# Optimization experiments

Hardware: AMD Instinct MI355X
Metric: run time of the kernel (lower is better)

## Reference

```python
import jax, jax.numpy as jnp
import numpy as np

ALPHA, GAMMA = 0.25, 2.0            # focal loss params (cfg defaults)
W_CLASS, W_BBOX, W_GIOU = 2.0, 5.0, 2.0
N_CANDIDATE_K = 5                   # top-k ious used to derive dynamic k
CENTER_RADIUS = 2.5
B, Q, G, C = 32, 2000, 64, 80
IMG_W, IMG_H = 1333.0, 800.0


def _box_iou(a, b):
    # a: [Q,4] xyxy, b: [G,4] xyxy -> iou [Q,G], union [Q,G]
    area_a = (a[:, 2] - a[:, 0]) * (a[:, 3] - a[:, 1])
    area_b = (b[:, 2] - b[:, 0]) * (b[:, 3] - b[:, 1])
    lt = jnp.maximum(a[:, None, :2], b[None, :, :2])
    rb = jnp.minimum(a[:, None, 2:], b[None, :, 2:])
    wh = jnp.clip(rb - lt, 0.0)
    inter = wh[..., 0] * wh[..., 1]
    union = area_a[:, None] + area_b[None, :] - inter
    return inter / union, union


def _generalized_box_iou(a, b):
    iou, union = _box_iou(a, b)
    lt = jnp.minimum(a[:, None, :2], b[None, :, :2])
    rb = jnp.maximum(a[:, None, 2:], b[None, :, 2:])
    wh = jnp.clip(rb - lt, 0.0)
    area_c = wh[..., 0] * wh[..., 1]
    return iou - (area_c - union) / area_c


def _get_in_boxes_info(boxes, gt):
    # boxes, gt: absolute xyxy. Anchor centers inside gt box / inside center region.
    cx = (boxes[:, 0] + boxes[:, 2]) * 0.5
    cy = (boxes[:, 1] + boxes[:, 3]) * 0.5
    is_in_boxes = ((cx[:, None] > gt[None, :, 0]) & (cx[:, None] < gt[None, :, 2]) &
                   (cy[:, None] > gt[None, :, 1]) & (cy[:, None] < gt[None, :, 3]))
    gt_cx = (gt[:, 0] + gt[:, 2]) * 0.5
    gt_cy = (gt[:, 1] + gt[:, 3]) * 0.5
    gt_w = gt[:, 2] - gt[:, 0]
    gt_h = gt[:, 3] - gt[:, 1]
    is_in_centers = ((cx[:, None] > (gt_cx - CENTER_RADIUS * gt_w)[None, :]) &
                     (cx[:, None] < (gt_cx + CENTER_RADIUS * gt_w)[None, :]) &
                     (cy[:, None] > (gt_cy - CENTER_RADIUS * gt_h)[None, :]) &
                     (cy[:, None] < (gt_cy + CENTER_RADIUS * gt_h)[None, :]))
    fg_mask = is_in_boxes.any(1) | is_in_centers.any(1)
    return fg_mask, is_in_boxes & is_in_centers


def _dedup(cost, matching):
    # queries matched to >1 gt keep only their min-cost gt
    over = matching.sum(1) > 1
    keep = jax.nn.one_hot(jnp.argmin(cost, axis=1), cost.shape[1], dtype=matching.dtype)
    return jnp.where(over[:, None], keep, matching)


def _dynamic_k_matching(cost, ious):
    Qn, Gn = cost.shape
    topk_ious = jax.lax.top_k(ious.T, N_CANDIDATE_K)[0]              # [G,k]
    dynamic_ks = jnp.maximum(topk_ious.sum(1).astype(jnp.int32), 1)  # [G]
    # rank of each query within each gt's cost column (ascending)
    ranks = jnp.argsort(jnp.argsort(cost, axis=0), axis=0)
    matching = (ranks < dynamic_ks[None, :]).astype(cost.dtype)      # [Q,G]
    matching = _dedup(cost, matching)

    # ensure every gt gets >=1 query; bounded loop replaces data-dependent while
    def body(_, carry):
        cost_c, match_c = carry
        unmatched = match_c.sum(0) == 0                              # [G]
        any_un = unmatched.any()
        matched_q = match_c.sum(1) > 0
        cost_n = cost_c + jnp.where(matched_q, 1e5, 0.0)[:, None]
        add = jax.nn.one_hot(jnp.argmin(cost_n, axis=0), Qn, dtype=match_c.dtype).T
        match_n = jnp.maximum(match_c, add * unmatched[None, :].astype(match_c.dtype))
        match_n = _dedup(cost_n, match_n)
        return (jnp.where(any_un, cost_n, cost_c), jnp.where(any_un, match_n, match_c))

    cost, matching = jax.lax.fori_loop(0, Gn, body, (cost, matching))
    masked = jnp.where(matching > 0, cost, jnp.inf)
    matched_query_id = jnp.argmin(masked, axis=0)                    # [G]
    return matching, matched_query_id


def _match_one(logits, boxes, tgt_ids, gt_boxes, size_out, size_tgt):
    fg_mask, in_bc = _get_in_boxes_info(boxes, gt_boxes)
    ious, _ = _box_iou(boxes, gt_boxes)                              # [Q,G]
    neg = (1.0 - ALPHA) * logits ** GAMMA * (-jnp.log(1.0 - logits + 1e-8))
    pos = ALPHA * (1.0 - logits) ** GAMMA * (-jnp.log(logits + 1e-8))
    cost_class = jnp.take(pos - neg, tgt_ids, axis=1)                # [Q,G]
    out_n = boxes / size_out                                         # [Q,4]
    tgt_n = gt_boxes / size_tgt                                      # [G,4]
    cost_bbox = jnp.abs(out_n[:, None, :] - tgt_n[None, :, :]).sum(-1)  # L1 cdist
    cost_giou = -_generalized_box_iou(boxes, gt_boxes)
    cost = (W_BBOX * cost_bbox + W_CLASS * cost_class + W_GIOU * cost_giou
            + 100.0 * (~in_bc).astype(cost_bbox.dtype))
    cost = cost + jnp.where(fg_mask, 0.0, 1e4)[:, None]
    return _dynamic_k_matching(cost, ious)


def _rand_boxes(key, n_shape):
    k1, k2 = jax.random.split(key)
    wh = jnp.array([IMG_W, IMG_H], jnp.float32)
    ctr = jax.random.uniform(k1, n_shape + (2,)) * wh
    size = jax.random.uniform(k2, n_shape + (2,)) * (wh * 0.3) + 8.0
    x1y1 = jnp.clip(ctr - size * 0.5, 0.0, wh)
    x2y2 = jnp.clip(ctr + size * 0.5, 0.0, wh)
    x2y2 = jnp.maximum(x2y2, x1y1 + 1.0)
    return jnp.concatenate([x1y1, x2y2], axis=-1)


def setup_inputs() -> dict:
    key = jax.random.key(0)
    k1, k2, k3, k4 = jax.random.split(key, 4)
    pred_logits = jax.random.uniform(k1, (B, Q, C), minval=1e-4, maxval=1.0 - 1e-4)
    pred_boxes = _rand_boxes(k2, (B, Q))
    gt_classes = jax.random.randint(k3, (B, G), 0, C)
    gt_boxes = _rand_boxes(k4, (B, G))
    sz = jnp.array([IMG_W, IMG_H, IMG_W, IMG_H], jnp.float32)
    return {
        'pred_logits': pred_logits,
        'pred_boxes': pred_boxes,
        'gt_classes': gt_classes,
        'gt_boxes': gt_boxes,
        'image_size_xyxy': jnp.tile(sz, (B, 1)),
        'image_size_xyxy_tgt': jnp.tile(sz, (B, G, 1)),
    }


def reference(pred_logits, pred_boxes, gt_classes, gt_boxes, image_size_xyxy, image_size_xyxy_tgt):
    # matching: [B,Q,G] 0/1 assignment matrix (row q matched to gt g);
    # matched_query_id: [B,G] best query per gt. Padded-G, fixed-shape analog of
    # the per-image variable-length (indices, matched_ids) lists.
    matching, matched_query_id = jax.vmap(_match_one)(
        pred_logits, pred_boxes, gt_classes, gt_boxes, image_size_xyxy, image_size_xyxy_tgt)
    return matching, matched_query_id
```

## Files before the change

kernel.cpp:

```cpp
#include <hip/hip_runtime.h>
#include <cmath>

#pragma clang fp contract(off)

#define BB 32
#define QQ 2000
#define GG 64
#define CCH 80
#define TOPC 16
#define QT 32

typedef unsigned long long u64;

__global__ __launch_bounds__(256) void cost_kernel(
    const float* __restrict__ logits, const float* __restrict__ boxes,
    const int* __restrict__ gtc, const float* __restrict__ gtb,
    const float* __restrict__ szout, const float* __restrict__ sztgt,
    float* __restrict__ cost, int* __restrict__ rowarg,
    float* __restrict__ out_match) {
#pragma clang fp contract(off)
  const int b = blockIdx.y;
  const int q0 = blockIdx.x * QT;
  const int t = threadIdx.x;
  const int w = t >> 6, lane = t & 63;

  __shared__ float4 s_qb[QT];
  __shared__ float4 s_qn[QT];
  __shared__ float s_tile[QT * 65];

  const int gbase = (b * GG + lane) * 4;
  const float g0 = gtb[gbase + 0], g1 = gtb[gbase + 1];
  const float g2 = gtb[gbase + 2], g3 = gtb[gbase + 3];
  const float t0 = g0 / sztgt[gbase + 0], t1 = g1 / sztgt[gbase + 1];
  const float t2 = g2 / sztgt[gbase + 2], t3 = g3 / sztgt[gbase + 3];
  const float garea = (g2 - g0) * (g3 - g1);
  const float gcx = (g0 + g2) * 0.5f, gcy = (g1 + g3) * 0.5f;
  const float gw = g2 - g0, gh = g3 - g1;
  const float cxlo = gcx - 2.5f * gw, cxhi = gcx + 2.5f * gw;
  const float cylo = gcy - 2.5f * gh, cyhi = gcy + 2.5f * gh;
  const int cls = gtc[b * GG + lane];

  if (t < QT) {
    int q = q0 + t;
    float4 bx = (q < QQ) ? reinterpret_cast<const float4*>(boxes)[b * QQ + q]
                         : make_float4(0.f, 0.f, 1.f, 1.f);
    s_qb[t] = bx;
    float4 on;
    on.x = bx.x / szout[b * 4 + 0];
    on.y = bx.y / szout[b * 4 + 1];
    on.z = bx.z / szout[b * 4 + 2];
    on.w = bx.w / szout[b * 4 + 3];
    s_qn[t] = on;
  }

  const float* lbase = logits + (size_t)b * QQ * CCH;
  float pv[8];
  #pragma unroll
  for (int i = 0; i < 8; ++i) {
    int q = q0 + w * 8 + i;
    pv[i] = (q < QQ) ? lbase[(size_t)q * CCH + cls] : 0.5f;
  }
  __syncthreads();

  #pragma unroll
  for (int i = 0; i < 8; ++i) {
    const int qi = w * 8 + i;
    float4 bx = s_qb[qi];
    float4 on = s_qn[qi];
    float x1 = bx.x, y1 = bx.y, x2 = bx.z, y2 = bx.w;
    float cx = (x1 + x2) * 0.5f, cy = (y1 + y2) * 0.5f;
    float areaa = (x2 - x1) * (y2 - y1);

    bool ib = (cx > g0) & (cx < g2) & (cy > g1) & (cy < g3);
    bool ic = (cx > cxlo) & (cx < cxhi) & (cy > cylo) & (cy < cyhi);
    bool fg = (__ballot(ib) != 0ull) || (__ballot(ic) != 0ull);
    float fgadd = fg ? 0.0f : 1e4f;

    float ltx = fmaxf(x1, g0), lty = fmaxf(y1, g1);
    float rbx = fminf(x2, g2), rby = fminf(y2, g3);
    float iw = fmaxf(rbx - ltx, 0.0f), ih = fmaxf(rby - lty, 0.0f);
    float inter = iw * ih;
    float uni = (areaa + garea) - inter;
    float iou = inter / uni;
    float ex1 = fminf(x1, g0), ey1 = fminf(y1, g1);
    float ex2 = fmaxf(x2, g2), ey2 = fmaxf(y2, g3);
    float ew = fmaxf(ex2 - ex1, 0.0f), eh = fmaxf(ey2 - ey1, 0.0f);
    float areac = ew * eh;
    float giou = iou - (areac - uni) / areac;

    float p = pv[i];
    float negc = (0.75f * (p * p)) * (-logf((1.0f - p) + 1e-8f));
    float posc = (0.25f * ((1.0f - p) * (1.0f - p))) * (-logf(p + 1e-8f));
    float ccls = posc - negc;

    float cb = ((fabsf(on.x - t0) + fabsf(on.y - t1)) + fabsf(on.z - t2)) + fabsf(on.w - t3);
    float notbc = (ib & ic) ? 0.0f : 1.0f;
    float c = ((5.0f * cb + 2.0f * ccls) + 2.0f * (-giou)) + 100.0f * notbc;
    c = c + fgadd;

    s_tile[qi * 65 + lane] = c;
  }
  __syncthreads();

  if (t < QT) {
    int q = q0 + t;
    if (q < QQ) {
      const float* row = &s_tile[t * 65];
      float bv = row[0]; int bg = 0;
      #pragma unroll
      for (int g = 1; g < GG; ++g) {
        float cv = row[g];
        if (cv < bv) { bv = cv; bg = g; }
      }
      rowarg[b * QQ + q] = bg;
    }
  }

  float* cb_out = cost + (size_t)b * GG * QQ;
  const int qi = t & 31;
  const int q = q0 + qi;
  if (q < QQ) {
    #pragma unroll
    for (int pass = 0; pass < 8; ++pass) {
      int g = (t >> 5) + pass * 8;
      cb_out[(size_t)g * QQ + q] = s_tile[qi * 65 + g];
    }
  }

  int nq = QQ - q0; if (nq > QT) nq = QT;
  if (nq > 0) {
    float4* zb = reinterpret_cast<float4*>(out_match + ((size_t)b * QQ + q0) * GG);
    int n4 = nq * GG / 4;
    float4 z = make_float4(0.f, 0.f, 0.f, 0.f);
    for (int i = t; i < n4; i += 256) zb[i] = z;
  }
}

template <int TOPN>
__device__ __forceinline__ void block_select(
    u64 (&K)[8], int tid, u64* s_tmin, u64* s_cmin, u64* s_surv,
    u64* s_sorted, u64* s_thr, int* s_ns) {
  u64 m = K[0];
  #pragma unroll
  for (int j = 1; j < 8; ++j) m = (K[j] < m) ? K[j] : m;
  s_tmin[tid] = m;
  if (tid == 0) *s_ns = 0;
  __syncthreads();

  if (tid < 64) {
    u64 c = s_tmin[tid];
    u64 c1 = s_tmin[tid + 64], c2 = s_tmin[tid + 128], c3 = s_tmin[tid + 192];
    c = (c1 < c) ? c1 : c; c = (c2 < c) ? c2 : c; c = (c3 < c) ? c3 : c;
    s_cmin[tid] = c;
    int r = 0;
    for (int j = 0; j < 64; ++j) r += (s_cmin[j] < c) ? 1 : 0;
    if (r == TOPN - 1) *s_thr = c;
  }
  __syncthreads();

  const u64 t = *s_thr;
  int n = 0;
  #pragma unroll
  for (int j = 0; j < 8; ++j) n += (K[j] <= t) ? 1 : 0;
  if (n) {
    int base = atomicAdd(s_ns, n);
    int k = 0;
    #pragma unroll
    for (int j = 0; j < 8; ++j) if (K[j] <= t) s_surv[base + (k++)] = K[j];
  }
  __syncthreads();

  const int ns = *s_ns;
  if (ns <= 64) {
    if (tid < ns && tid < 64) {
      u64 k = s_surv[tid];
      int r = 0;
      for (int j = 0; j < ns; ++j) r += (s_surv[j] < k) ? 1 : 0;
      if (r < TOPN) s_sorted[r] = k;
    }
  } else if (tid < 64) {
    for (int pass = 0; pass < TOPN; ++pass) {
      u64 bk = ~0ull;
      for (int idx = tid; idx < ns; idx += 64) {
        u64 v = s_surv[idx]; bk = (v < bk) ? v : bk;
      }
      for (int off = 32; off; off >>= 1) {
        u64 ok = __shfl_down(bk, off, 64); bk = (ok < bk) ? ok : bk;
      }
      bk = __shfl(bk, 0, 64);
      for (int idx = tid; idx < ns; idx += 64)
        if (s_surv[idx] == bk) s_surv[idx] = ~0ull;
      if (tid == 0) s_sorted[pass] = bk;
    }
  }
  __syncthreads();
}

__global__ __launch_bounds__(256) void pick_kernel(
    const float* __restrict__ boxes, const float* __restrict__ gtb,
    const float* __restrict__ cost, short* __restrict__ lists,
    int* __restrict__ dynks) {
#pragma clang fp contract(off)
  const int bc = blockIdx.x;
  const int b = bc >> 6, col = bc & 63;
  const int tid = threadIdx.x;

  __shared__ u64 s_tmin[256];
  __shared__ u64 s_cmin[64];
  __shared__ u64 s_surv[512];
  __shared__ u64 s_sorted[TOPC];
  __shared__ u64 s_thr;
  __shared__ int s_ns;

  const int gbase = (b * GG + col) * 4;
  const float gx1 = gtb[gbase + 0], gy1 = gtb[gbase + 1];
  const float gx2 = gtb[gbase + 2], gy2 = gtb[gbase + 3];
  const float ga = (gx2 - gx1) * (gy2 - gy1);

  u64 K[8];
  #pragma unroll
  for (int j = 0; j < 8; ++j) {
    int q = tid * 8 + j;
    float val = -1e30f;
    if (q < QQ) {
      float4 bx = reinterpret_cast<const float4*>(boxes)[b * QQ + q];
      float areaa = (bx.z - bx.x) * (bx.w - bx.y);
      float ltx = fmaxf(bx.x, gx1), lty = fmaxf(bx.y, gy1);
      float rbx = fminf(bx.z, gx2), rby = fminf(bx.w, gy2);
      float iw = fmaxf(rbx - ltx, 0.0f), ih = fmaxf(rby - lty, 0.0f);
      float inter = iw * ih;
      val = inter / ((areaa + ga) - inter);
    }
    unsigned u = __float_as_uint(val);
    u = (u & 0x80000000u) ? ~u : (u | 0x80000000u);
    K[j] = ~(((u64)u << 16) | (u64)(0xFFFF - q));
  }
  block_select<5>(K, tid, s_tmin, s_cmin, s_surv, s_sorted, &s_thr, &s_ns);
  if (tid == 0) {
    float s = 0.0f;
    for (int r = 0; r < 5; ++r) {
      u64 kk = ~s_sorted[r];
      unsigned u = (unsigned)(kk >> 16);
      u = (u & 0x80000000u) ? (u & 0x7FFFFFFFu) : ~u;
      s += __uint_as_float(u);
    }
    int dynk = (int)s;
    if (dynk < 1) dynk = 1;
    dynks[bc] = dynk;
  }

  const float* ccol = cost + (size_t)bc * QQ;
  {
    float cv[8];
    if (tid < 249) {
      const float4* c4 = reinterpret_cast<const float4*>(ccol) + tid * 2;
      float4 a = c4[0], d = c4[1];
      cv[0] = a.x; cv[1] = a.y; cv[2] = a.z; cv[3] = a.w;
      cv[4] = d.x; cv[5] = d.y; cv[6] = d.z; cv[7] = d.w;
    } else {
      #pragma unroll
      for (int j = 0; j < 8; ++j) {
        int q = tid * 8 + j;
        cv[j] = (q < QQ) ? ccol[q] : INFINITY;
      }
    }
    #pragma unroll
    for (int j = 0; j < 8; ++j) {
      unsigned u = __float_as_uint(cv[j]);
      u = (u & 0x80000000u) ? ~u : (u | 0x80000000u);
      K[j] = ((u64)u << 16) | (u64)(tid * 8 + j);
    }
  }
  block_select<TOPC>(K, tid, s_tmin, s_cmin, s_surv, s_sorted, &s_thr, &s_ns);
  if (tid < TOPC) lists[bc * TOPC + tid] = (short)(s_sorted[tid] & 0xFFFFull);
}

__global__ __launch_bounds__(256) void serial_kernel(
    const float* __restrict__ cost, const short* __restrict__ lists,
    const int* __restrict__ dynks, const int* __restrict__ rowarg,
    float* __restrict__ out_match, float* __restrict__ out_ids) {
#pragma clang fp contract(off)
  const int b = blockIdx.x;
  const int tid = threadIdx.x;

  __shared__ unsigned s_mlo[QQ], s_mhi[QQ];
  __shared__ int s_first[QQ];
  __shared__ unsigned char s_mq[QQ];
  __shared__ short s_rarg[QQ];
  __shared__ int s_cnt[GG];
  __shared__ u64 s_pack[GG];
  __shared__ int s_added[GG];
  __shared__ int s_nadd, s_Tv;

  for (int q = tid; q < QQ; q += 256) {
    s_mlo[q] = 0u; s_mhi[q] = 0u; s_first[q] = -1; s_mq[q] = 0;
    s_rarg[q] = (short)rowarg[b * QQ + q];
  }
  if (tid < GG) s_cnt[tid] = 0;
  __syncthreads();

  if (tid < GG) {
    int dynk = dynks[b * GG + tid];
    s_cnt[tid] = dynk;
    const short* lrow = lists + (b * GG + tid) * TOPC;
    for (int i = 0; i < dynk; ++i) {
      int q = lrow[i];
      if (tid < 32) atomicOr(&s_mlo[q], 1u << tid);
      else          atomicOr(&s_mhi[q], 1u << (tid - 32));
      s_first[q] = 0;
      s_mq[q] = 1;
    }
  }
  __syncthreads();

  for (int q = tid; q < QQ; q += 256) {
    unsigned lo = s_mlo[q], hi = s_mhi[q];
    if (__popc(lo) + __popc(hi) > 1) {
      int bg = s_rarg[q];
      unsigned tl = lo, th = hi;
      while (tl) { int g = __ffs(tl) - 1; tl &= tl - 1; if (g != bg) atomicSub(&s_cnt[g], 1); }
      while (th) { int g = __ffs(th) + 31; th &= th - 1; if (g != bg) atomicSub(&s_cnt[g], 1); }
      bool had = (bg < 32) ? ((lo >> bg) & 1u) : ((hi >> (bg - 32)) & 1u);
      if (!had) atomicAdd(&s_cnt[bg], 1);
      s_mlo[q] = (bg < 32) ? (1u << bg) : 0u;
      s_mhi[q] = (bg >= 32) ? (1u << (bg - 32)) : 0u;
    }
  }
  __syncthreads();

  const float* costb = cost + (size_t)b * GG * QQ;

  if (tid < 64) {
    const int lane = tid;
    unsigned cand[8];
    {
      const unsigned* lrow =
          reinterpret_cast<const unsigned*>(lists + (b * GG + lane) * TOPC);
      #pragma unroll
      for (int j = 0; j < 8; ++j) cand[j] = lrow[j];
    }
    int T = 0;
    for (int iter = 0; iter < GG; ++iter) {
      unsigned long long bal = __ballot(s_cnt[lane] > 0);
      unsigned long long um = ~bal;
      if (um == 0ull) break;
      T++;
      bool isun = (um >> lane) & 1ull;
      if (lane == 0) s_nadd = 0;

      int myq = -1;
      unsigned fmask = 0;
      if (isun) {
        #pragma unroll
        for (int i = 0; i < 16; ++i) {
          int cq = (cand[i >> 1] >> (16 * (i & 1))) & 0xFFFF;
          fmask |= ((unsigned)(s_mq[cq] == 0)) << i;
        }
        if (fmask) {
          int idx = __ffs(fmask) - 1;
          myq = (cand[idx >> 1] >> (16 * (idx & 1))) & 0xFFFF;
        }
      }

      unsigned long long fb = __ballot(isun && fmask == 0);
      while (fb) {
        int col = __ffsll(fb) - 1; fb &= fb - 1;
        const float* ccol = costb + (size_t)col * QQ;
        float bv = INFINITY; int bq = 0x7fffffff;
        for (int q2 = lane; q2 < QQ; q2 += 64) {
          if (s_mq[q2] == 0) {
            float cv = ccol[q2];
            if (cv < bv) { bv = cv; bq = q2; }
          }
        }
        for (int off = 32; off; off >>= 1) {
          float ov = __shfl_down(bv, off, 64); int oq = __shfl_down(bq, off, 64);
          if (ov < bv || (ov == bv && oq < bq)) { bv = ov; bq = oq; }
        }
        bq = __shfl(bq, 0, 64);
        if (bq == 0x7fffffff) {
          bv = INFINITY; bq = 0x7fffffff;
          for (int q2 = lane; q2 < QQ; q2 += 64) {
            float cv = ccol[q2];
            int k = (s_first[q2] >= 0) ? (iter + 1 - s_first[q2]) : 0;
            for (int tt = 0; tt < k; ++tt) cv += 1e5f;
            if (cv < bv) { bv = cv; bq = q2; }
          }
          for (int off = 32; off; off >>= 1) {
            float ov = __shfl_down(bv, off, 64); int oq = __shfl_down(bq, off, 64);
            if (ov < bv || (ov == bv && oq < bq)) { bv = ov; bq = oq; }
          }
          bq = __shfl(bq, 0, 64);
        }
        if (lane == col) myq = bq;
      }

      if (isun) {
        int q = myq;
        if (lane < 32) atomicOr(&s_mlo[q], 1u << lane);
        else           atomicOr(&s_mhi[q], 1u << (lane - 32));
        atomicAdd(&s_cnt[lane], 1);
        if (s_first[q] < 0) s_first[q] = iter + 1;
        s_mq[q] = 1;
        int slot = atomicAdd(&s_nadd, 1);
        s_added[slot] = q;
      }

      int na = s_nadd;
      if (lane < na) {
        int q = s_added[lane];
        bool dup = false;
        for (int j = 0; j < lane; ++j) dup = dup || (s_added[j] == q);
        if (!dup) {
          unsigned lo = s_mlo[q], hi = s_mhi[q];
          if (__popc(lo) + __popc(hi) > 1) {
            int bg = s_rarg[q];
            unsigned tl = lo, th = hi;
            while (tl) { int g = __ffs(tl) - 1; tl &= tl - 1; if (g != bg) atomicSub(&s_cnt[g], 1); }
            while (th) { int g = __ffs(th) + 31; th &= th - 1; if (g != bg) atomicSub(&s_cnt[g], 1); }
            bool had = (bg < 32) ? ((lo >> bg) & 1u) : ((hi >> (bg - 32)) & 1u);
            if (!had) atomicAdd(&s_cnt[bg], 1);
            s_mlo[q] = (bg < 32) ? (1u << bg) : 0u;
            s_mhi[q] = (bg >= 32) ? (1u << (bg - 32)) : 0u;
          }
        }
      }
    }
    if (tid == 0) s_Tv = T;
  }
  __syncthreads();
  const int T = s_Tv;

  if (tid < GG) s_pack[tid] = 0xFFFFFFFFFFFFFFFFull;
  __syncthreads();
  for (int q = tid; q < QQ; q += 256) {
    unsigned lo = s_mlo[q], hi = s_mhi[q];
    if (lo | hi) {
      int g = lo ? (__ffs(lo) - 1) : (__ffs(hi) + 31);
      float cv = costb[(size_t)g * QQ + q];
      int k = T - s_first[q];
      for (int tt = 0; tt < k; ++tt) cv += 1e5f;
      unsigned ub = __float_as_uint(cv);
      ub = (ub & 0x80000000u) ? ~ub : (ub | 0x80000000u);
      u64 pk = ((u64)ub << 16) | (unsigned)q;
      atomicMin(&s_pack[g], pk);
    }
  }
  __syncthreads();
  if (tid < GG) {
    u64 pk = s_pack[tid];
    out_ids[b * GG + tid] =
        (pk == 0xFFFFFFFFFFFFFFFFull) ? 0.0f : (float)(pk & 0xFFFFull);
  }
  for (int q = tid; q < QQ; q += 256) {
    unsigned lo = s_mlo[q], hi = s_mhi[q];
    if (lo | hi) {
      int g = lo ? (__ffs(lo) - 1) : (__ffs(hi) + 31);
      out_match[((size_t)b * QQ + q) * GG + g] = 1.0f;
    }
  }
}

extern "C" void kernel_launch(void* const* d_in, const int* in_sizes, int n_in,
                              void* d_out, int out_size, void* d_ws, size_t ws_size,
                              hipStream_t stream) {
  const float* logits = (const float*)d_in[0];
  const float* boxes  = (const float*)d_in[1];
  const int*   gtc    = (const int*)d_in[2];
  const float* gtbx   = (const float*)d_in[3];
  const float* szout  = (const float*)d_in[4];
  const float* sztgt  = (const float*)d_in[5];
  float* out = (float*)d_out;

  const size_t matchN  = (size_t)BB * QQ * GG;
  const size_t rowargN = (size_t)BB * QQ;
  const size_t listsN  = (size_t)BB * GG * TOPC;

  char* p = (char*)d_ws;
  float* cost   = (float*)p;          p += matchN * 4;
  int*   rowarg = (int*)p;            p += rowargN * 4;
  short* lists  = (short*)p;          p += listsN * 2;
  int*   dynks  = (int*)p;

  float* out_ids = out + matchN;

  hipLaunchKernelGGL(cost_kernel, dim3((QQ + QT - 1) / QT, BB), dim3(256), 0, stream,
                     logits, boxes, gtc, gtbx, szout, sztgt, cost, rowarg, out);
  hipLaunchKernelGGL(pick_kernel, dim3(BB * GG), dim3(256), 0, stream,
                     boxes, gtbx, cost, lists, dynks);
  hipLaunchKernelGGL(serial_kernel, dim3(BB), dim3(256), 0, stream,
                     cost, lists, dynks, rowarg, out, out_ids);
}
```

Measured before the change: 127.0 us.

## Fuse three kernels into one cooperative persistent kernel with grid syncs

```diff
diff --git a/kernel.cpp b/kernel.cpp
--- a/kernel.cpp
+++ b/kernel.cpp
@@ -1,7 +1,10 @@
 #include <hip/hip_runtime.h>
+#include <hip/hip_cooperative_groups.h>
 #include <cmath>
 
 #pragma clang fp contract(off)
+
+namespace cg = cooperative_groups;
 
 #define BB 32
 #define QQ 2000
@@ -12,21 +15,76 @@
 
 typedef unsigned long long u64;
 
-__global__ __launch_bounds__(256) void cost_kernel(
+template <int TOPN>
+__device__ __forceinline__ void block_select_raw(
+    u64 (&K)[8], int tid, u64* s_tmin, u64* s_cmin, u64* s_surv,
+    u64* s_sorted, u64* s_thr, int* s_ns) {
+  u64 m = K[0];
+  #pragma unroll
+  for (int j = 1; j < 8; ++j) m = (K[j] < m) ? K[j] : m;
+  s_tmin[tid] = m;
+  if (tid == 0) *s_ns = 0;
+  __syncthreads();
+
+  if (tid < 64) {
+    u64 c = s_tmin[tid];
+    u64 c1 = s_tmin[tid + 64], c2 = s_tmin[tid + 128], c3 = s_tmin[tid + 192];
+    c = (c1 < c) ? c1 : c; c = (c2 < c) ? c2 : c; c = (c3 < c) ? c3 : c;
+    s_cmin[tid] = c;
+    int r = 0;
+    for (int j = 0; j < 64; ++j) r += (s_cmin[j] < c) ? 1 : 0;
+    if (r == TOPN - 1) *s_thr = c;
+  }
+  __syncthreads();
+
+  const u64 t = *s_thr;
+  int n = 0;
+  #pragma unroll
+  for (int j = 0; j < 8; ++j) n += (K[j] <= t) ? 1 : 0;
+  if (n) {
+    int base = atomicAdd(s_ns, n);
+    int k = 0;
+    #pragma unroll
+    for (int j = 0; j < 8; ++j) if (K[j] <= t) s_surv[base + (k++)] = K[j];
+  }
+  __syncthreads();
+
+  const int ns = *s_ns;
+  if (ns <= 64) {
+    if (tid < ns && tid < 64) {
+      u64 k = s_surv[tid];
+      int r = 0;
+      for (int j = 0; j < ns; ++j) r += (s_surv[j] < k) ? 1 : 0;
+      if (r < TOPN) s_sorted[r] = k;
+    }
+  } else if (tid < 64) {
+    for (int pass = 0; pass < TOPN; ++pass) {
+      u64 bk = ~0ull;
+      for (int idx = tid; idx < ns; idx += 64) {
+        u64 v = s_surv[idx]; bk = (v < bk) ? v : bk;
+      }
+      for (int off = 32; off; off >>= 1) {
+        u64 ok = __shfl_down(bk, off, 64); bk = (ok < bk) ? ok : bk;
+      }
+      bk = __shfl(bk, 0, 64);
+      for (int idx = tid; idx < ns; idx += 64)
+        if (s_surv[idx] == bk) s_surv[idx] = ~0ull;
+      if (tid == 0) s_sorted[pass] = bk;
+    }
+  }
+  __syncthreads();
+}
+
+__device__ __forceinline__ void cost_job(
+    int b, int q0, int tid,
     const float* __restrict__ logits, const float* __restrict__ boxes,
     const int* __restrict__ gtc, const float* __restrict__ gtb,
     const float* __restrict__ szout, const float* __restrict__ sztgt,
     float* __restrict__ cost, int* __restrict__ rowarg,
-    float* __restrict__ out_match) {
+    float* __restrict__ out_match,
+    float4* s_qb, float4* s_qn, float* s_tile) {
 #pragma clang fp contract(off)
-  const int b = blockIdx.y;
-  const int q0 = blockIdx.x * QT;
-  const int t = threadIdx.x;
-  const int w = t >> 6, lane = t & 63;
-
-  __shared__ float4 s_qb[QT];
-  __shared__ float4 s_qn[QT];
-  __shared__ float s_tile[QT * 65];
+  const int w = tid >> 6, lane = tid & 63;
 
   const int gbase = (b * GG + lane) * 4;
   const float g0 = gtb[gbase + 0], g1 = gtb[gbase + 1];
@@ -40,17 +98,17 @@
   const float cylo = gcy - 2.5f * gh, cyhi = gcy + 2.5f * gh;
   const int cls = gtc[b * GG + lane];
 
-  if (t < QT) {
-    int q = q0 + t;
+  if (tid < QT) {
+    int q = q0 + tid;
     float4 bx = (q < QQ) ? reinterpret_cast<const float4*>(boxes)[b * QQ + q]
                          : make_float4(0.f, 0.f, 1.f, 1.f);
-    s_qb[t] = bx;
+    s_qb[tid] = bx;
     float4 on;
     on.x = bx.x / szout[b * 4 + 0];
     on.y = bx.y / szout[b * 4 + 1];
     on.z = bx.z / szout[b * 4 + 2];
     on.w = bx.w / szout[b * 4 + 3];
-    s_qn[t] = on;
+    s_qn[tid] = on;
   }
 
   const float* lbase = logits + (size_t)b * QQ * CCH;
@@ -102,10 +160,10 @@
   }
   __syncthreads();
 
-  if (t < QT) {
-    int q = q0 + t;
+  if (tid < QT) {
+    int q = q0 + tid;
     if (q < QQ) {
-      const float* row = &s_tile[t * 65];
+      const float* row = &s_tile[tid * 65];
       float bv = row[0]; int bg = 0;
       #pragma unroll
       for (int g = 1; g < GG; ++g) {
@@ -117,12 +175,12 @@
   }
 
   float* cb_out = cost + (size_t)b * GG * QQ;
-  const int qi = t & 31;
+  const int qi = tid & 31;
   const int q = q0 + qi;
   if (q < QQ) {
     #pragma unroll
     for (int pass = 0; pass < 8; ++pass) {
-      int g = (t >> 5) + pass * 8;
+      int g = (tid >> 5) + pass * 8;
       cb_out[(size_t)g * QQ + q] = s_tile[qi * 65 + g];
     }
   }
@@ -132,86 +190,19 @@
     float4* zb = reinterpret_cast<float4*>(out_match + ((size_t)b * QQ + q0) * GG);
     int n4 = nq * GG / 4;
     float4 z = make_float4(0.f, 0.f, 0.f, 0.f);
-    for (int i = t; i < n4; i += 256) zb[i] = z;
-  }
-}
-
-template <int TOPN>
-__device__ __forceinline__ void block_select(
-    u64 (&K)[8], int tid, u64* s_tmin, u64* s_cmin, u64* s_surv,
-    u64* s_sorted, u64* s_thr, int* s_ns) {
-  u64 m = K[0];
-  #pragma unroll
-  for (int j = 1; j < 8; ++j) m = (K[j] < m) ? K[j] : m;
-  s_tmin[tid] = m;
-  if (tid == 0) *s_ns = 0;
-  __syncthreads();
-
-  if (tid < 64) {
-    u64 c = s_tmin[tid];
-    u64 c1 = s_tmin[tid + 64], c2 = s_tmin[tid + 128], c3 = s_tmin[tid + 192];
-    c = (c1 < c) ? c1 : c; c = (c2 < c) ? c2 : c; c = (c3 < c) ? c3 : c;
-    s_cmin[tid] = c;
-    int r = 0;
-    for (int j = 0; j < 64; ++j) r += (s_cmin[j] < c) ? 1 : 0;
-    if (r == TOPN - 1) *s_thr = c;
-  }
-  __syncthreads();
-
-  const u64 t = *s_thr;
-  int n = 0;
-  #pragma unroll
-  for (int j = 0; j < 8; ++j) n += (K[j] <= t) ? 1 : 0;
-  if (n) {
-    int base = atomicAdd(s_ns, n);
-    int k = 0;
-    #pragma unroll
-    for (int j = 0; j < 8; ++j) if (K[j] <= t) s_surv[base + (k++)] = K[j];
-  }
-  __syncthreads();
-
-  const int ns = *s_ns;
-  if (ns <= 64) {
-    if (tid < ns && tid < 64) {
-      u64 k = s_surv[tid];
-      int r = 0;
-      for (int j = 0; j < ns; ++j) r += (s_surv[j] < k) ? 1 : 0;
-      if (r < TOPN) s_sorted[r] = k;
-    }
-  } else if (tid < 64) {
-    for (int pass = 0; pass < TOPN; ++pass) {
-      u64 bk = ~0ull;
-      for (int idx = tid; idx < ns; idx += 64) {
-        u64 v = s_surv[idx]; bk = (v < bk) ? v : bk;
-      }
-      for (int off = 32; off; off >>= 1) {
-        u64 ok = __shfl_down(bk, off, 64); bk = (ok < bk) ? ok : bk;
-      }
-      bk = __shfl(bk, 0, 64);
-      for (int idx = tid; idx < ns; idx += 64)
-        if (s_surv[idx] == bk) s_surv[idx] = ~0ull;
-      if (tid == 0) s_sorted[pass] = bk;
-    }
-  }
-  __syncthreads();
-}
-
-__global__ __launch_bounds__(256) void pick_kernel(
+    for (int i2 = tid; i2 < n4; i2 += 256) zb[i2] = z;
+  }
+  __syncthreads();
+}
+
+__device__ __forceinline__ void pick_job(
+    int bc, int tid,
     const float* __restrict__ boxes, const float* __restrict__ gtb,
     const float* __restrict__ cost, short* __restrict__ lists,
-    int* __restrict__ dynks) {
+    int* __restrict__ dynks,
+    u64* s_tmin, u64* s_cmin, u64* s_surv, u64* s_sorted, u64* s_thr, int* s_ns) {
 #pragma clang fp contract(off)
-  const int bc = blockIdx.x;
   const int b = bc >> 6, col = bc & 63;
-  const int tid = threadIdx.x;
-
-  __shared__ u64 s_tmin[256];
-  __shared__ u64 s_cmin[64];
-  __shared__ u64 s_surv[512];
-  __shared__ u64 s_sorted[TOPC];
-  __shared__ u64 s_thr;
-  __shared__ int s_ns;
-
   const int gbase = (b * GG + col) * 4;
   const float gx1 = gtb[gbase + 0], gy1 = gtb[gbase + 1];
   const float gx2 = gtb[gbase + 2], gy2 = gtb[gbase + 3];
@@ -235,7 +226,7 @@
     u = (u & 0x80000000u) ? ~u : (u | 0x80000000u);
     K[j] = ~(((u64)u << 16) | (u64)(0xFFFF - q));
   }
-  block_select<5>(K, tid, s_tmin, s_cmin, s_surv, s_sorted, &s_thr, &s_ns);
+  block_select_raw<5>(K, tid, s_tmin, s_cmin, s_surv, s_sorted, s_thr, s_ns);
   if (tid == 0) {
     float s = 0.0f;
     for (int r = 0; r < 5; ++r) {
@@ -271,59 +262,60 @@
       K[j] = ((u64)u << 16) | (u64)(tid * 8 + j);
     }
   }
-  block_select<TOPC>(K, tid, s_tmin, s_cmin, s_surv, s_sorted, &s_thr, &s_ns);
+  block_select_raw<TOPC>(K, tid, s_tmin, s_cmin, s_surv, s_sorted, s_thr, s_ns);
   if (tid < TOPC) lists[bc * TOPC + tid] = (short)(s_sorted[tid] & 0xFFFFull);
-}
-
-__global__ __launch_bounds__(256) void serial_kernel(
+  __syncthreads();
+}
+
+struct SerialLds {
+  unsigned mlo[QQ], mhi[QQ];
+  short first[QQ];
+  unsigned char mq[QQ];
+  short rarg[QQ];
+  int cnt[GG];
+  u64 pack[GG];
+  int added[GG];
+  int nadd, Tv;
+};
+
+__device__ __forceinline__ void serial_job(
+    int b, int tid, SerialLds* sp,
     const float* __restrict__ cost, const short* __restrict__ lists,
     const int* __restrict__ dynks, const int* __restrict__ rowarg,
     float* __restrict__ out_match, float* __restrict__ out_ids) {
 #pragma clang fp contract(off)
-  const int b = blockIdx.x;
-  const int tid = threadIdx.x;
-
-  __shared__ unsigned s_mlo[QQ], s_mhi[QQ];
-  __shared__ int s_first[QQ];
-  __shared__ unsigned char s_mq[QQ];
-  __shared__ short s_rarg[QQ];
-  __shared__ int s_cnt[GG];
-  __shared__ u64 s_pack[GG];
-  __shared__ int s_added[GG];
-  __shared__ int s_nadd, s_Tv;
-
   for (int q = tid; q < QQ; q += 256) {
-    s_mlo[q] = 0u; s_mhi[q] = 0u; s_first[q] = -1; s_mq[q] = 0;
-    s_rarg[q] = (short)rowarg[b * QQ + q];
-  }
-  if (tid < GG) s_cnt[tid] = 0;
+    sp->mlo[q] = 0u; sp->mhi[q] = 0u; sp->first[q] = -1; sp->mq[q] = 0;
+    sp->rarg[q] = (short)rowarg[b * QQ + q];
+  }
+  if (tid < GG) sp->cnt[tid] = 0;
   __syncthreads();
 
   if (tid < GG) {
     int dynk = dynks[b * GG + tid];
-    s_cnt[tid] = dynk;
+    sp->cnt[tid] = dynk;
     const short* lrow = lists + (b * GG + tid) * TOPC;
     for (int i = 0; i < dynk; ++i) {
       int q = lrow[i];
-      if (tid < 32) atomicOr(&s_mlo[q], 1u << tid);
-      else          atomicOr(&s_mhi[q], 1u << (tid - 32));
-      s_first[q] = 0;
-      s_mq[q] = 1;
+      if (tid < 32) atomicOr(&sp->mlo[q], 1u << tid);
+      else          atomicOr(&sp->mhi[q], 1u << (tid - 32));
+      sp->first[q] = 0;
+      sp->mq[q] = 1;
     }
   }
   __syncthreads();
 
   for (int q = tid; q < QQ; q += 256) {
-    unsigned lo = s_mlo[q], hi = s_mhi[q];
+    unsigned lo = sp->mlo[q], hi = sp->mhi[q];
     if (__popc(lo) + __popc(hi) > 1) {
-      int bg = s_rarg[q];
+      int bg = sp->rarg[q];
       unsigned tl = lo, th = hi;
-      while (tl) { int g = __ffs(tl) - 1; tl &= tl - 1; if (g != bg) atomicSub(&s_cnt[g], 1); }
-      while (th) { int g = __ffs(th) + 31; th &= th - 1; if (g != bg) atomicSub(&s_cnt[g], 1); }
+      while (tl) { int g = __ffs(tl) - 1; tl &= tl - 1; if (g != bg) atomicSub(&sp->cnt[g], 1); }
+      while (th) { int g = __ffs(th) + 31; th &= th - 1; if (g != bg) atomicSub(&sp->cnt[g], 1); }
       bool had = (bg < 32) ? ((lo >> bg) & 1u) : ((hi >> (bg - 32)) & 1u);
-      if (!had) atomicAdd(&s_cnt[bg], 1);
-      s_mlo[q] = (bg < 32) ? (1u << bg) : 0u;
-      s_mhi[q] = (bg >= 32) ? (1u << (bg - 32)) : 0u;
+      if (!had) atomicAdd(&sp->cnt[bg], 1);
+      sp->mlo[q] = (bg < 32) ? (1u << bg) : 0u;
+      sp->mhi[q] = (bg >= 32) ? (1u << (bg - 32)) : 0u;
     }
   }
   __syncthreads();
@@ -341,12 +333,12 @@
     }
     int T = 0;
     for (int iter = 0; iter < GG; ++iter) {
-      unsigned long long bal = __ballot(s_cnt[lane] > 0);
+      unsigned long long bal = __ballot(sp->cnt[lane] > 0);
       unsigned long long um = ~bal;
       if (um == 0ull) break;
       T++;
       bool isun = (um >> lane) & 1ull;
-      if (lane == 0) s_nadd = 0;
+      if (lane == 0) sp->nadd = 0;
 
       int myq = -1;
       unsigned fmask = 0;
@@ -354,7 +346,7 @@
         #pragma unroll
         for (int i = 0; i < 16; ++i) {
           int cq = (cand[i >> 1] >> (16 * (i & 1))) & 0xFFFF;
-          fmask |= ((unsigned)(s_mq[cq] == 0)) << i;
+          fmask |= ((unsigned)(sp->mq[cq] == 0)) << i;
         }
         if (fmask) {
           int idx = __ffs(fmask) - 1;
@@ -368,7 +360,7 @@
         const float* ccol = costb + (size_t)col * QQ;
         float bv = INFINITY; int bq = 0x7fffffff;
         for (int q2 = lane; q2 < QQ; q2 += 64) {
-          if (s_mq[q2] == 0) {
+          if (sp->mq[q2] == 0) {
             float cv = ccol[q2];
             if (cv < bv) { bv = cv; bq = q2; }
           }
@@ -382,7 +374,7 @@
           bv = INFINITY; bq = 0x7fffffff;
           for (int q2 = lane; q2 < QQ; q2 += 64) {
             float cv = ccol[q2];
-            int k = (s_first[q2] >= 0) ? (iter + 1 - s_first[q2]) : 0;
+            int k = (sp->first[q2] >= 0) ? (iter + 1 - sp->first[q2]) : 0;
             for (int tt = 0; tt < k; ++tt) cv += 1e5f;
             if (cv < bv) { bv = cv; bq = q2; }
           }
@@ -397,68 +389,129 @@
 
       if (isun) {
         int q = myq;
-        if (lane < 32) atomicOr(&s_mlo[q], 1u << lane);
-        else           atomicOr(&s_mhi[q], 1u << (lane - 32));
-        atomicAdd(&s_cnt[lane], 1);
-        if (s_first[q] < 0) s_first[q] = iter + 1;
-        s_mq[q] = 1;
-        int slot = atomicAdd(&s_nadd, 1);
-        s_added[slot] = q;
-      }
-
-      int na = s_nadd;
+        if (lane < 32) atomicOr(&sp->mlo[q], 1u << lane);
+        else           atomicOr(&sp->mhi[q], 1u << (lane - 32));
+        atomicAdd(&sp->cnt[lane], 1);
+        if (sp->first[q] < 0) sp->first[q] = (short)(iter + 1);
+        sp->mq[q] = 1;
+        int slot = atomicAdd(&sp->nadd, 1);
+        sp->added[slot] = q;
+      }
+
+      int na = sp->nadd;
       if (lane < na) {
-        int q = s_added[lane];
+        int q = sp->added[lane];
         bool dup = false;
-        for (int j = 0; j < lane; ++j) dup = dup || (s_added[j] == q);
+        for (int j = 0; j < lane; ++j) dup = dup || (sp->added[j] == q);
         if (!dup) {
-          unsigned lo = s_mlo[q], hi = s_mhi[q];
+          unsigned lo = sp->mlo[q], hi = sp->mhi[q];
           if (__popc(lo) + __popc(hi) > 1) {
-            int bg = s_rarg[q];
+            int bg = sp->rarg[q];
             unsigned tl = lo, th = hi;
-            while (tl) { int g = __ffs(tl) - 1; tl &= tl - 1; if (g != bg) atomicSub(&s_cnt[g], 1); }
-            while (th) { int g = __ffs(th) + 31; th &= th - 1; if (g != bg) atomicSub(&s_cnt[g], 1); }
+            while (tl) { int g = __ffs(tl) - 1; tl &= tl - 1; if (g != bg) atomicSub(&sp->cnt[g], 1); }
+            while (th) { int g = __ffs(th) + 31; th &= th - 1; if (g != bg) atomicSub(&sp->cnt[g], 1); }
             bool had = (bg < 32) ? ((lo >> bg) & 1u) : ((hi >> (bg - 32)) & 1u);
-            if (!had) atomicAdd(&s_cnt[bg], 1);
-            s_mlo[q] = (bg < 32) ? (1u << bg) : 0u;
-            s_mhi[q] = (bg >= 32) ? (1u << (bg - 32)) : 0u;
+            if (!had) atomicAdd(&sp->cnt[bg], 1);
+            sp->mlo[q] = (bg < 32) ? (1u << bg) : 0u;
+            sp->mhi[q] = (bg >= 32) ? (1u << (bg - 32)) : 0u;
           }
         }
       }
     }
-    if (tid == 0) s_Tv = T;
-  }
-  __syncthreads();
-  const int T = s_Tv;
-
-  if (tid < GG) s_pack[tid] = 0xFFFFFFFFFFFFFFFFull;
+    if (tid == 0) sp->Tv = T;
+  }
+  __syncthreads();
+  const int T = sp->Tv;
+
+  if (tid < GG) sp->pack[tid] = 0xFFFFFFFFFFFFFFFFull;
   __syncthreads();
   for (int q = tid; q < QQ; q += 256) {
-    unsigned lo = s_mlo[q], hi = s_mhi[q];
+    unsigned lo = sp->mlo[q], hi = sp->mhi[q];
     if (lo | hi) {
       int g = lo ? (__ffs(lo) - 1) : (__ffs(hi) + 31);
       float cv = costb[(size_t)g * QQ + q];
-      int k = T - s_first[q];
+      int k = T - sp->first[q];
       for (int tt = 0; tt < k; ++tt) cv += 1e5f;
       unsigned ub = __float_as_uint(cv);
       ub = (ub & 0x80000000u) ? ~ub : (ub | 0x80000000u);
       u64 pk = ((u64)ub << 16) | (unsigned)q;
-      atomicMin(&s_pack[g], pk);
+      atomicMin(&sp->pack[g], pk);
     }
   }
   __syncthreads();
   if (tid < GG) {
-    u64 pk = s_pack[tid];
+    u64 pk = sp->pack[tid];
     out_ids[b * GG + tid] =
         (pk == 0xFFFFFFFFFFFFFFFFull) ? 0.0f : (float)(pk & 0xFFFFull);
   }
   for (int q = tid; q < QQ; q += 256) {
-    unsigned lo = s_mlo[q], hi = s_mhi[q];
+    unsigned lo = sp->mlo[q], hi = sp->mhi[q];
     if (lo | hi) {
       int g = lo ? (__ffs(lo) - 1) : (__ffs(hi) + 31);
       out_match[((size_t)b * QQ + q) * GG + g] = 1.0f;
     }
   }
+}
+
+struct P1Lds { float4 qb[QT]; float4 qn[QT]; float tile[QT * 65]; };
+struct P2Lds { u64 tmin[256]; u64 cmin[64]; u64 surv[512]; u64 sorted[TOPC]; u64 thr; int ns; };
+
+__global__ __launch_bounds__(256, 2) void mono_kernel(
+    const float* __restrict__ logits, const float* __restrict__ boxes,
+    const int* __restrict__ gtc, const float* __restrict__ gtb,
+    const float* __restrict__ szout, const float* __restrict__ sztgt,
+    float* __restrict__ cost, int* __restrict__ rowarg,
+    short* __restrict__ lists, int* __restrict__ dynks,
+    float* __restrict__ out_match, float* __restrict__ out_ids) {
+  __shared__ __align__(16) union { P1Lds p1; P2Lds p2; SerialLds p3; } smem;
+  const int tid = threadIdx.x;
+
+  for (int job = blockIdx.x; job < 63 * BB; job += gridDim.x) {
+    cost_job(job / 63, (job % 63) * QT, tid, logits, boxes, gtc, gtb, szout,
+             sztgt, cost, rowarg, out_match, smem.p1.qb, smem.p1.qn, smem.p1.tile);
+  }
+  __threadfence();
+  cg::this_grid().sync();
+
+  for (int bc = blockIdx.x; bc < BB * GG; bc += gridDim.x) {
+    pick_job(bc, tid, boxes, gtb, cost, lists, dynks, smem.p2.tmin,
+             smem.p2.cmin, smem.p2.surv, smem.p2.sorted, &smem.p2.thr, &smem.p2.ns);
+  }
+  __threadfence();
+  cg::this_grid().sync();
+
+  if (blockIdx.x < BB)
+    serial_job(blockIdx.x, tid, &smem.p3, cost, lists, dynks, rowarg,
+               out_match, out_ids);
+}
+
+__global__ __launch_bounds__(256) void cost_kernel(
+    const float* __restrict__ logits, const float* __restrict__ boxes,
+    const int* __restrict__ gtc, const float* __restrict__ gtb,
+    const float* __restrict__ szout, const float* __restrict__ sztgt,
+    float* __restrict__ cost, int* __restrict__ rowarg,
+    float* __restrict__ out_match) {
+  __shared__ __align__(16) P1Lds s;
+  cost_job(blockIdx.y, blockIdx.x * QT, threadIdx.x, logits, boxes, gtc, gtb,
+           szout, sztgt, cost, rowarg, out_match, s.qb, s.qn, s.tile);
+}
+
+__global__ __launch_bounds__(256) void pick_kernel(
+    const float* __restrict__ boxes, const float* __restrict__ gtb,
+    const float* __restrict__ cost, short* __restrict__ lists,
+    int* __restrict__ dynks) {
+  __shared__ __align__(16) P2Lds s;
+  pick_job(blockIdx.x, threadIdx.x, boxes, gtb, cost, lists, dynks,
+           s.tmin, s.cmin, s.surv, s.sorted, &s.thr, &s.ns);
+}
+
+__global__ __launch_bounds__(256) void serial_kernel(
+    const float* __restrict__ cost, const short* __restrict__ lists,
+    const int* __restrict__ dynks, const int* __restrict__ rowarg,
+    float* __restrict__ out_match, float* __restrict__ out_ids) {
+  __shared__ __align__(16) SerialLds s;
+  serial_job(blockIdx.x, threadIdx.x, &s, cost, lists, dynks, rowarg,
+             out_match, out_ids);
 }
 
 extern "C" void kernel_launch(void* const* d_in, const int* in_sizes, int n_in,
@@ -484,10 +537,32 @@
 
   float* out_ids = out + matchN;
 
-  hipLaunchKernelGGL(cost_kernel, dim3((QQ + QT - 1) / QT, BB), dim3(256), 0, stream,
-                     logits, boxes, gtc, gtbx, szout, sztgt, cost, rowarg, out);
-  hipLaunchKernelGGL(pick_kernel, dim3(BB * GG), dim3(256), 0, stream,
-                     boxes, gtbx, cost, lists, dynks);
-  hipLaunchKernelGGL(serial_kernel, dim3(BB), dim3(256), 0, stream,
-                     cost, lists, dynks, rowarg, out, out_ids);
-}
+  int nb = 0;
+  hipError_t oe = hipOccupancyMaxActiveBlocksPerMultiprocessor(
+      &nb, (const void*)mono_kernel, 256, 0);
+  bool ok = (oe == hipSuccess) && (nb >= 1);
+  if (ok) {
+    int grid = 256 * nb;
+    if (grid > 512) grid = 512;
+    if (grid < BB) ok = false;
+    if (ok) {
+      void* args[] = {
+        (void*)&logits, (void*)&boxes, (void*)&gtc, (void*)&gtbx,
+        (void*)&szout, (void*)&sztgt, (void*)&cost, (void*)&rowarg,
+        (void*)&lists, (void*)&dynks, (void*)&out, (void*)&out_ids,
+      };
+      hipError_t le = hipLaunchCooperativeKernel(
+          (const void*)mono_kernel, dim3(grid), dim3(256), args, 0, stream);
+      if (le != hipSuccess) ok = false;
+    }
+  }
+  if (!ok) {
+    hipLaunchKernelGGL(cost_kernel, dim3((QQ + QT - 1) / QT, BB), dim3(256), 0,
+                       stream, logits, boxes, gtc, gtbx, szout, sztgt, cost,
+                       rowarg, out);
+    hipLaunchKernelGGL(pick_kernel, dim3(BB * GG), dim3(256), 0, stream,
+                       boxes, gtbx, cost, lists, dynks);
+    hipLaunchKernelGGL(serial_kernel, dim3(BB), dim3(256), 0, stream,
+                       cost, lists, dynks, rowarg, out, out_ids);
+  }
+}
```

Result: slower. 333.2 us (+162.3%).
